# Performance work log

Hardware: AMD Instinct MI355X
Metric: run time of the kernel (lower is better)

The kernel has to match this reference:

```python
import jax, jax.numpy as jnp
import numpy as np

MAX_ITERS = 50
EPS_NORM = 1e-8
EPS_SEP = -1e-6


def setup_inputs() -> dict:
    key = jax.random.key(0)
    k1, k2 = jax.random.split(key)
    pointcloud = jax.random.normal(k1, (200000, 3), dtype=jnp.float32)
    targets = jax.random.normal(k2, (256, 3), dtype=jnp.float32)
    return {"pointcloud": pointcloud, "targets": targets}


def reference(pointcloud, targets):
    # pointcloud: [N, d], targets: [M, d]
    N = pointcloud.shape[0]
    M = targets.shape[0]
    p2 = jnp.sum(pointcloud * pointcloud, axis=1)  # [N]
    t2 = jnp.sum(targets * targets, axis=1)        # [M]

    def step(mask, _):
        # squared euclidean distances [M, N] (argmin identical to cdist argmin)
        d2 = t2[:, None] + p2[None, :] - 2.0 * (targets @ pointcloud.T)
        d2 = jnp.where(mask, d2, jnp.inf)
        closest_idx = jnp.argmin(d2, axis=1)           # [M]
        closest_points = pointcloud[closest_idx]       # [M, d]
        a = closest_points - targets
        a = a / (jnp.linalg.norm(a, axis=1, keepdims=True) + EPS_NORM)
        b = jnp.sum(a * closest_points, axis=1)        # [M]
        dot = a @ pointcloud.T - b[:, None]            # [M, N]
        separated = dot >= EPS_SEP
        mask = mask & ~separated
        return mask, (a, b)

    mask0 = jnp.ones((M, N), dtype=bool)
    _, (a_stack, b_stack) = jax.lax.scan(step, mask0, None, length=MAX_ITERS)
    return a_stack, b_stack  # [MAX_ITERS, M, d], [MAX_ITERS, M]
```

## Files before the change

### kernel.cpp

```cpp
#include <hip/hip_runtime.h>
#include <stdint.h>
#include <math.h>

#pragma clang fp contract(off)

#define BLOCK 1024
#define NW (BLOCK / 64)
#define PT 8
#define PB 4
#define MAX_ITERS 50
#define SOLO_CAP 2048
#define EPS_NORM 1e-8f
#define EPS_SEP (-1e-6f)

__global__ __launch_bounds__(BLOCK) void convex_plane_kernel(
    const float* __restrict__ pc, const float* __restrict__ tg,
    float* __restrict__ out, int N, int M, int CAP, int stepsA)
{
    extern __shared__ uint32_t smem[];
    const int tid  = threadIdx.x;
    const int lane = tid & 63;
    const int wv   = tid >> 6;
    const int m    = blockIdx.x;

    const int maskW = stepsA * (PT * BLOCK / 32);
    uint32_t* mask  = smem;
    int*      list  = (int*)(smem + maskW);
    float*    red_d = (float*)(list + CAP);
    int*      red_i = (int*)(red_d + NW);
    int*      cw    = red_i + NW;
    int*      bcast = cw + NW;
    int*      cnt   = bcast + 2;

    const float tx = tg[3*m+0], ty = tg[3*m+1], tz = tg[3*m+2];
    const float t2 = tx*tx + ty*ty + tz*tz;

    float* out_a = out;
    float* out_b = out + (size_t)MAX_ITERS * (size_t)M * 3;

    auto ldp = [&](int ip, float& x, float& y, float& z) {
        const float* p = pc + 3 * (size_t)ip;
        x = p[0]; y = p[1]; z = p[2];
    };

    auto finish = [&](float dmin, int imin, int mycnt, bool cntFromCursor) -> int2 {
        #pragma unroll
        for (int off = 32; off > 0; off >>= 1) {
            float od = __shfl_down(dmin, off, 64);
            int   oi = __shfl_down(imin, off, 64);
            int   oc = __shfl_down(mycnt, off, 64);
            if (od < dmin || (od == dmin && oi < imin)) { dmin = od; imin = oi; }
            mycnt += oc;
        }
        if (lane == 0) { red_d[wv] = dmin; red_i[wv] = imin; cw[wv] = mycnt; }
        __syncthreads();
        if (wv == 0) {
            float bd = (lane < NW) ? red_d[lane] : INFINITY;
            int   bi = (lane < NW) ? red_i[lane] : 0;
            int   c  = (lane < NW) ? cw[lane]    : 0;
            #pragma unroll
            for (int off = 8; off > 0; off >>= 1) {
                float od = __shfl_down(bd, off, 64);
                int   oi = __shfl_down(bi, off, 64);
                int   oc = __shfl_down(c,  off, 64);
                if (od < bd || (od == bd && oi < bi)) { bd = od; bi = oi; }
                c += oc;
            }
            if (lane == 0) { bcast[0] = bi; bcast[1] = cntFromCursor ? cnt[0] : c; }
        }
        __syncthreads();
        int2 r; r.x = bcast[0]; r.y = bcast[1];
        return r;
    };

    auto scanA = [&](int mode, bool build,
                     float ax, float ay, float az, float b) -> int2 {
        if (tid == 0) cnt[0] = 0;
        __syncthreads();
        float dmin = INFINITY;
        int   imin = 0;
        int   mycnt = 0;
        for (int s = 0; s < stepsA; ++s) {
            const int ib    = s * PT * BLOCK + tid;
            const int wbase = s * (PT * BLOCK / 32);
            uint32_t live = 0;
            if (mode == 2) {
                #pragma unroll
                for (int j = 0; j < PT; ++j) {
                    uint32_t w = mask[wbase + j * (BLOCK / 32) + (tid >> 5)];
                    live |= ((w >> (tid & 31)) & 1u) << j;
                }
            } else {
                #pragma unroll
                for (int j = 0; j < PT; ++j)
                    if (ib + j * BLOCK < N) live |= (1u << j);
            }
            float px[PT], py[PT], pz[PT];
            #pragma unroll
            for (int j = 0; j < PT; ++j) {
                int ip = ib + j * BLOCK;
                ip = ip < N ? ip : N - 1;
                const float* p = pc + 3 * (size_t)ip;
                px[j] = p[0]; py[j] = p[1]; pz[j] = p[2];
            }
            uint32_t keepm = 0;
            #pragma unroll
            for (int j = 0; j < PT; ++j) {
                if ((live >> j) & 1u) {
                    bool keep;
                    if (mode == 0) keep = true;
                    else {
                        float dt = ax*px[j] + ay*py[j] + az*pz[j] - b;
                        keep = (dt < EPS_SEP);
                    }
                    if (keep) {
                        keepm |= (1u << j);
                        float p2 = px[j]*px[j] + py[j]*py[j] + pz[j]*pz[j];
                        float tp = tx*px[j] + ty*py[j] + tz*pz[j];
                        float d2 = t2 + p2 - 2.0f*tp;
                        const int i = ib + j * BLOCK;
                        if (d2 < dmin || (d2 == dmin && i < imin)) {
                            dmin = d2; imin = i;
                        }
                    }
                }
            }
            if (mode != 0) {
                #pragma unroll
                for (int j = 0; j < PT; ++j) {
                    unsigned long long bal = __ballot(((keepm >> j) & 1u) != 0u);
                    const int widx = wbase + j * (BLOCK / 32) + (wv << 1);
                    if (lane == 0)       mask[widx]     = (uint32_t)bal;
                    else if (lane == 32) mask[widx + 1] = (uint32_t)(bal >> 32);
                }
            }
            mycnt += (int)__popc(keepm);
            if (build) {
                int c = (int)__popc(keepm);
                int incl = c;
                #pragma unroll
                for (int off = 1; off < 64; off <<= 1) {
                    int o = __shfl_up(incl, off, 64);
                    if (lane >= off) incl += o;
                }
                const int excl = incl - c;
                const int tot  = __shfl(incl, 63, 64);
                int wb = 0;
                if (lane == 0) wb = atomicAdd(cnt, tot);
                wb = __shfl(wb, 0, 64);
                int pos = wb + excl;
                #pragma unroll
                for (int j = 0; j < PT; ++j) {
                    if ((keepm >> j) & 1u) {
                        if (pos < CAP) list[pos] = ib + j * BLOCK;
                        ++pos;
                    }
                }
            }
        }
        return finish(dmin, imin, mycnt, false);
    };

    auto scanB = [&](int count, float ax, float ay, float az, float b) -> int2 {
        if (tid == 0) cnt[0] = 0;
        __syncthreads();
        float dmin = INFINITY;
        int   imin = 0;
        const int per = BLOCK * PB;
        const int bsteps = (count + per - 1) / per;
        for (int s = 0; s < bsteps; ++s) {
            int jv[PB]; float xv[PB], yv[PB], zv[PB];
            #pragma unroll
            for (int q = 0; q < PB; ++q) {
                int e = s * per + q * BLOCK + tid;
                e = e < count ? e : count - 1;
                jv[q] = list[e];
            }
            #pragma unroll
            for (int q = 0; q < PB; ++q)
                ldp(jv[q], xv[q], yv[q], zv[q]);
            uint32_t keepm = 0;
            float d2v[PB];
            #pragma unroll
            for (int q = 0; q < PB; ++q) {
                const int e = s * per + q * BLOCK + tid;
                if (e < count) {
                    float dt = ax*xv[q] + ay*yv[q] + az*zv[q] - b;
                    if (dt < EPS_SEP) {
                        keepm |= (1u << q);
                        float p2 = xv[q]*xv[q] + yv[q]*yv[q] + zv[q]*zv[q];
                        float tp = tx*xv[q] + ty*yv[q] + tz*zv[q];
                        d2v[q] = t2 + p2 - 2.0f*tp;
                    }
                }
            }
            __syncthreads();
            int c = (int)__popc(keepm);
            int incl = c;
            #pragma unroll
            for (int off = 1; off < 64; off <<= 1) {
                int o = __shfl_up(incl, off, 64);
                if (lane >= off) incl += o;
            }
            const int excl = incl - c;
            const int tot  = __shfl(incl, 63, 64);
            int wb = 0;
            if (lane == 0) wb = atomicAdd(cnt, tot);
            wb = __shfl(wb, 0, 64);
            int pos = wb + excl;
            #pragma unroll
            for (int q = 0; q < PB; ++q) {
                if ((keepm >> q) & 1u) {
                    list[pos] = jv[q];
                    if (d2v[q] < dmin || (d2v[q] == dmin && jv[q] < imin)) {
                        dmin = d2v[q]; imin = jv[q];
                    }
                    ++pos;
                }
            }
        }
        __syncthreads();
        return finish(dmin, imin, 0, true);
    };

    bool comp = false;
    int2 rc = scanA(0, false, 0.f, 0.f, 0.f, 0.f);
    int idx = rc.x, count = rc.y;

    for (int k = 0; k < MAX_ITERS; ++k) {
        if (comp && count <= SOLO_CAP) {
            float* lx = (float*)(list + SOLO_CAP);
            float* ly = lx + SOLO_CAP;
            float* lz = ly + SOLO_CAP;
            for (int e = tid; e < count; e += BLOCK) {
                float x, y, z;
                ldp(list[e], x, y, z);
                lx[e] = x; ly[e] = y; lz[e] = z;
            }
            __syncthreads();
            if (wv != 0) return;
            for (; k < MAX_ITERS; ++k) {
                float cx, cy, cz;
                ldp(idx, cx, cy, cz);
                const float vx = cx - tx, vy = cy - ty, vz = cz - tz;
                const float nrm = sqrtf(vx*vx + vy*vy + vz*vz);
                const float den = nrm + EPS_NORM;
                const float ax = vx / den, ay = vy / den, az = vz / den;
                const float b  = ax*cx + ay*cy + az*cz;
                if (count == 0) {
                    for (int q = lane; q < MAX_ITERS - k; q += 64) {
                        const int kk = k + q;
                        const size_t oa = ((size_t)kk * M + m) * 3;
                        out_a[oa+0] = ax; out_a[oa+1] = ay; out_a[oa+2] = az;
                        out_b[(size_t)kk * M + m] = b;
                    }
                    return;
                }
                if (lane == 0) {
                    const size_t oa = ((size_t)k * M + m) * 3;
                    out_a[oa+0] = ax; out_a[oa+1] = ay; out_a[oa+2] = az;
                    out_b[(size_t)k * M + m] = b;
                }
                if (k + 1 < MAX_ITERS) {
                    float dmin = INFINITY; int imin = 0; int wcur = 0;
                    for (int e0 = 0; e0 < count; e0 += 64) {
                        const int e = e0 + lane;
                        bool keep = false; int j = 0;
                        float d2v = 0.f, px = 0.f, py = 0.f, pz = 0.f;
                        if (e < count) {
                            j = list[e];
                            px = lx[e]; py = ly[e]; pz = lz[e];
                            float dt = ax*px + ay*py + az*pz - b;
                            if (dt < EPS_SEP) {
                                keep = true;
                                float p2 = px*px + py*py + pz*pz;
                                float tp = tx*px + ty*py + tz*pz;
                                d2v = t2 + p2 - 2.0f*tp;
                            }
                        }
                        unsigned long long bal = __ballot(keep);
                        int pos = wcur + (int)__popcll(bal & ((1ull << lane) - 1ull));
                        if (keep) {
                            list[pos] = j;
                            lx[pos] = px; ly[pos] = py; lz[pos] = pz;
                            if (d2v < dmin || (d2v == dmin && j < imin)) {
                                dmin = d2v; imin = j;
                            }
                        }
                        wcur += (int)__popcll(bal);
                    }
                    #pragma unroll
                    for (int off = 32; off > 0; off >>= 1) {
                        float od = __shfl_down(dmin, off, 64);
                        int   oi = __shfl_down(imin, off, 64);
                        if (od < dmin || (od == dmin && oi < imin)) { dmin = od; imin = oi; }
                    }
                    idx = __shfl(imin, 0, 64);
                    count = wcur;
                }
            }
            return;
        }

        float cx, cy, cz;
        ldp(idx, cx, cy, cz);
        const float vx = cx - tx, vy = cy - ty, vz = cz - tz;
        const float nrm = sqrtf(vx*vx + vy*vy + vz*vz);
        const float den = nrm + EPS_NORM;
        const float ax = vx / den, ay = vy / den, az = vz / den;
        const float b  = ax*cx + ay*cy + az*cz;

        if (count == 0) {
            for (int q = tid; q < MAX_ITERS - k; q += BLOCK) {
                const int kk = k + q;
                const size_t oa = ((size_t)kk * M + m) * 3;
                out_a[oa+0] = ax; out_a[oa+1] = ay; out_a[oa+2] = az;
                out_b[(size_t)kk * M + m] = b;
            }
            return;
        }
        if (tid == 0) {
            const size_t oa = ((size_t)k * M + m) * 3;
            out_a[oa+0] = ax; out_a[oa+1] = ay; out_a[oa+2] = az;
            out_b[(size_t)k * M + m] = b;
        }
        if (k + 1 < MAX_ITERS) {
            if (comp) {
                rc = scanB(count, ax, ay, az, b);
            } else {
                const bool build = (count <= (5 * CAP) / 2);
                rc = scanA(k == 0 ? 1 : 2, build, ax, ay, az, b);
                if (build && rc.y <= CAP) comp = true;
            }
            idx = rc.x; count = rc.y;
        }
    }
}

extern "C" void kernel_launch(void* const* d_in, const int* in_sizes, int n_in,
                              void* d_out, int out_size, void* d_ws, size_t ws_size,
                              hipStream_t stream) {
    const float* pc = (const float*)d_in[0];
    const float* tg = (const float*)d_in[1];
    float* out = (float*)d_out;
    const int N = in_sizes[0] / 3;
    const int M = in_sizes[1] / 3;
    const int stepsA = (N + BLOCK * PT - 1) / (BLOCK * PT);
    const size_t maskB  = (size_t)stepsA * (PT * BLOCK / 32) * sizeof(uint32_t);
    const size_t fixedB = NW * (2 * sizeof(int) + sizeof(float)) + 3 * sizeof(int);

    int CAP = 32768;
    size_t smem = maskB + (size_t)CAP * sizeof(int) + fixedB;
    if (hipFuncSetAttribute((const void*)convex_plane_kernel,
                            hipFuncAttributeMaxDynamicSharedMemorySize,
                            (int)smem) != hipSuccess) {
        CAP = 8192;
        smem = maskB + (size_t)CAP * sizeof(int) + fixedB;
    }
    convex_plane_kernel<<<M, BLOCK, smem, stream>>>(pc, tg, out, N, M, CAP, stepsA);
}
```

Measured before the change: 547.5 us.

## Spatially sort points into Morton bins and skip dead wave chunks

Adds preprocessing kernels that histogram the points into a 16^3 Morton-ordered grid, scan the counts and scatter the points into a packed float4 buffer in the workspace, with the original index stored in w. The main kernel reads these packed points, remaps each wave to a contiguous chunk, and records per-chunk survivor counts so later passes skip chunks with no surviving points. Spatial locality should make whole chunks die together under the plane cuts, and the float4 layout gives single vector loads. The cost is several extra launches with atomics and more workspace, and correctness now depends on carrying original indices through for argmin tie-breaking.

```diff
diff --git a/kernel.cpp b/kernel.cpp
--- a/kernel.cpp
+++ b/kernel.cpp
@@ -10,11 +10,92 @@
 #define PB 4
 #define MAX_ITERS 50
 #define SOLO_CAP 2048
+#define NBINS 4096
 #define EPS_NORM 1e-8f
 #define EPS_SEP (-1e-6f)
 
+__device__ __forceinline__ int bin_of(float x, float y, float z) {
+    int cx = (int)floorf((x + 3.5f) * (16.0f / 7.0f));
+    int cy = (int)floorf((y + 3.5f) * (16.0f / 7.0f));
+    int cz = (int)floorf((z + 3.5f) * (16.0f / 7.0f));
+    cx = cx < 0 ? 0 : (cx > 15 ? 15 : cx);
+    cy = cy < 0 ? 0 : (cy > 15 ? 15 : cy);
+    cz = cz < 0 ? 0 : (cz > 15 ? 15 : cz);
+    int code = 0;
+    #pragma unroll
+    for (int b = 0; b < 4; ++b) {
+        code |= ((cx >> b) & 1) << (3 * b);
+        code |= ((cy >> b) & 1) << (3 * b + 1);
+        code |= ((cz >> b) & 1) << (3 * b + 2);
+    }
+    return code;
+}
+
+__global__ void zero_bins(int* __restrict__ binCnt) {
+    const int i = blockIdx.x * blockDim.x + threadIdx.x;
+    if (i < NBINS) binCnt[i] = 0;
+}
+
+__global__ void hist_bins(const float* __restrict__ pc, int* __restrict__ binCnt,
+                          int N) {
+    const int i = blockIdx.x * blockDim.x + threadIdx.x;
+    if (i < N)
+        atomicAdd(&binCnt[bin_of(pc[3*i+0], pc[3*i+1], pc[3*i+2])], 1);
+}
+
+__global__ void scan_bins(const int* __restrict__ binCnt,
+                          int* __restrict__ binCur) {
+    __shared__ int wsum[16];
+    const int t = threadIdx.x, lane = t & 63, wv = t >> 6;
+    const int v0 = binCnt[4*t+0], v1 = binCnt[4*t+1],
+              v2 = binCnt[4*t+2], v3 = binCnt[4*t+3];
+    const int s = v0 + v1 + v2 + v3;
+    int incl = s;
+    #pragma unroll
+    for (int off = 1; off < 64; off <<= 1) {
+        int o = __shfl_up(incl, off, 64);
+        if (lane >= off) incl += o;
+    }
+    if (lane == 63) wsum[wv] = incl;
+    __syncthreads();
+    if (t == 0) {
+        int acc = 0;
+        for (int w = 0; w < 16; ++w) { int x = wsum[w]; wsum[w] = acc; acc += x; }
+    }
+    __syncthreads();
+    const int excl = incl - s + wsum[wv];
+    binCur[4*t+0] = excl;
+    binCur[4*t+1] = excl + v0;
+    binCur[4*t+2] = excl + v0 + v1;
+    binCur[4*t+3] = excl + v0 + v1 + v2;
+}
+
+__global__ void scatter_bins(const float* __restrict__ pc,
+                             float4* __restrict__ pk,
+                             int* __restrict__ binCur, int N) {
+    const int i = blockIdx.x * blockDim.x + threadIdx.x;
+    if (i < N) {
+        const float x = pc[3*i+0], y = pc[3*i+1], z = pc[3*i+2];
+        const int pos = atomicAdd(&binCur[bin_of(x, y, z)], 1);
+        float4 v; v.x = x; v.y = y; v.z = z; v.w = __int_as_float(i);
+        pk[pos] = v;
+    }
+}
+
+__global__ void pack_identity(const float* __restrict__ pc,
+                              float4* __restrict__ pk, int N) {
+    const int i = blockIdx.x * blockDim.x + threadIdx.x;
+    if (i < N) {
+        float4 v; v.x = pc[3*i+0]; v.y = pc[3*i+1]; v.z = pc[3*i+2];
+        v.w = __int_as_float(i);
+        pk[i] = v;
+    }
+}
+
+template <bool PK>
 __global__ __launch_bounds__(BLOCK) void convex_plane_kernel(
-    const float* __restrict__ pc, const float* __restrict__ tg,
+    const float* __restrict__ pc, const float4* __restrict__ pk,
+    const float* __restrict__ tg,
     float* __restrict__ out, int N, int M, int CAP, int stepsA)
 {
     extern __shared__ uint32_t smem[];
@@ -31,17 +112,13 @@
     int*      cw    = red_i + NW;
     int*      bcast = cw + NW;
     int*      cnt   = bcast + 2;
+    int*      chk   = cnt + 1;
 
     const float tx = tg[3*m+0], ty = tg[3*m+1], tz = tg[3*m+2];
     const float t2 = tx*tx + ty*ty + tz*tz;
 
     float* out_a = out;
     float* out_b = out + (size_t)MAX_ITERS * (size_t)M * 3;
-
-    auto ldp = [&](int ip, float& x, float& y, float& z) {
-        const float* p = pc + 3 * (size_t)ip;
-        x = p[0]; y = p[1]; z = p[2];
-    };
 
     auto finish = [&](float dmin, int imin, int mycnt, bool cntFromCursor) -> int2 {
         #pragma unroll
@@ -81,32 +158,46 @@
         int   imin = 0;
         int   mycnt = 0;
         for (int s = 0; s < stepsA; ++s) {
-            const int ib    = s * PT * BLOCK + tid;
-            const int wbase = s * (PT * BLOCK / 32);
-            uint32_t live = 0;
+            const int cid = s * NW + wv;
+            if (mode == 2 && chk[cid] == 0) continue;
+            const int pbase = s * (PT * BLOCK) + wv * (PT * 64) + lane;
+            const int wwb   = s * (PT * BLOCK / 32) + wv * (PT * 2);
+            uint32_t livem = 0;
             if (mode == 2) {
                 #pragma unroll
                 for (int j = 0; j < PT; ++j) {
-                    uint32_t w = mask[wbase + j * (BLOCK / 32) + (tid >> 5)];
-                    live |= ((w >> (tid & 31)) & 1u) << j;
+                    uint32_t w = mask[wwb + j * 2 + (lane >> 5)];
+                    livem |= ((w >> (lane & 31)) & 1u) << j;
                 }
             } else {
                 #pragma unroll
                 for (int j = 0; j < PT; ++j)
-                    if (ib + j * BLOCK < N) live |= (1u << j);
-            }
-            float px[PT], py[PT], pz[PT];
+                    if (pbase + j * 64 < N) livem |= (1u << j);
+            }
+            float px[PT], py[PT], pz[PT]; int ov[PT];
+            if constexpr (PK) {
+                #pragma unroll
+                for (int j = 0; j < PT; ++j) {
+                    int ip = pbase + j * 64;
+                    ip = ip < N ? ip : N - 1;
+                    const float4 v = pk[ip];
+                    px[j] = v.x; py[j] = v.y; pz[j] = v.z;
+                    ov[j] = __float_as_int(v.w);
+                }
+            } else {
+                #pragma unroll
+                for (int j = 0; j < PT; ++j) {
+                    int ip = pbase + j * 64;
+                    ip = ip < N ? ip : N - 1;
+                    const float* p = pc + 3 * (size_t)ip;
+                    px[j] = p[0]; py[j] = p[1]; pz[j] = p[2];
+                    ov[j] = ip;
+                }
+            }
+            uint32_t keepm = 0;
             #pragma unroll
             for (int j = 0; j < PT; ++j) {
-                int ip = ib + j * BLOCK;
-                ip = ip < N ? ip : N - 1;
-                const float* p = pc + 3 * (size_t)ip;
-                px[j] = p[0]; py[j] = p[1]; pz[j] = p[2];
-            }
-            uint32_t keepm = 0;
-            #pragma unroll
-            for (int j = 0; j < PT; ++j) {
-                if ((live >> j) & 1u) {
+                if ((livem >> j) & 1u) {
                     bool keep;
                     if (mode == 0) keep = true;
                     else {
@@ -118,23 +209,26 @@
                         float p2 = px[j]*px[j] + py[j]*py[j] + pz[j]*pz[j];
                         float tp = tx*px[j] + ty*py[j] + tz*pz[j];
                         float d2 = t2 + p2 - 2.0f*tp;
-                        const int i = ib + j * BLOCK;
-                        if (d2 < dmin || (d2 == dmin && i < imin)) {
-                            dmin = d2; imin = i;
+                        if (d2 < dmin || (d2 == dmin && ov[j] < imin)) {
+                            dmin = d2; imin = ov[j];
                         }
                     }
                 }
             }
+            mycnt += (int)__popc(keepm);
             if (mode != 0) {
                 #pragma unroll
                 for (int j = 0; j < PT; ++j) {
                     unsigned long long bal = __ballot(((keepm >> j) & 1u) != 0u);
-                    const int widx = wbase + j * (BLOCK / 32) + (wv << 1);
-                    if (lane == 0)       mask[widx]     = (uint32_t)bal;
-                    else if (lane == 32) mask[widx + 1] = (uint32_t)(bal >> 32);
-                }
-            }
-            mycnt += (int)__popc(keepm);
+                    if (lane == 0)       mask[wwb + j*2]     = (uint32_t)bal;
+                    else if (lane == 32) mask[wwb + j*2 + 1] = (uint32_t)(bal >> 32);
+                }
+                int wsumc = (int)__popc(keepm);
+                #pragma unroll
+                for (int off = 32; off > 0; off >>= 1)
+                    wsumc += __shfl_down(wsumc, off, 64);
+                if (lane == 0) chk[cid] = wsumc;
+            }
             if (build) {
                 int c = (int)__popc(keepm);
                 int incl = c;
@@ -152,7 +246,7 @@
                 #pragma unroll
                 for (int j = 0; j < PT; ++j) {
                     if ((keepm >> j) & 1u) {
-                        if (pos < CAP) list[pos] = ib + j * BLOCK;
+                        if (pos < CAP) list[pos] = pbase + j * 64;
                         ++pos;
                     }
                 }
@@ -169,7 +263,7 @@
         const int per = BLOCK * PB;
         const int bsteps = (count + per - 1) / per;
         for (int s = 0; s < bsteps; ++s) {
-            int jv[PB]; float xv[PB], yv[PB], zv[PB];
+            int jv[PB]; float xv[PB], yv[PB], zv[PB]; int ov[PB]; float d2v[PB];
             #pragma unroll
             for (int q = 0; q < PB; ++q) {
                 int e = s * per + q * BLOCK + tid;
@@ -177,10 +271,18 @@
                 jv[q] = list[e];
             }
             #pragma unroll
-            for (int q = 0; q < PB; ++q)
-                ldp(jv[q], xv[q], yv[q], zv[q]);
+            for (int q = 0; q < PB; ++q) {
+                if constexpr (PK) {
+                    const float4 v = pk[jv[q]];
+                    xv[q] = v.x; yv[q] = v.y; zv[q] = v.z;
+                    ov[q] = __float_as_int(v.w);
+                } else {
+                    const float* p = pc + 3 * (size_t)jv[q];
+                    xv[q] = p[0]; yv[q] = p[1]; zv[q] = p[2];
+                    ov[q] = jv[q];
+                }
+            }
             uint32_t keepm = 0;
-            float d2v[PB];
             #pragma unroll
             for (int q = 0; q < PB; ++q) {
                 const int e = s * per + q * BLOCK + tid;
@@ -212,8 +314,8 @@
             for (int q = 0; q < PB; ++q) {
                 if ((keepm >> q) & 1u) {
                     list[pos] = jv[q];
-                    if (d2v[q] < dmin || (d2v[q] == dmin && jv[q] < imin)) {
-                        dmin = d2v[q]; imin = jv[q];
+                    if (d2v[q] < dmin || (d2v[q] == dmin && ov[q] < imin)) {
+                        dmin = d2v[q]; imin = ov[q];
                     }
                     ++pos;
                 }
@@ -233,15 +335,20 @@
             float* ly = lx + SOLO_CAP;
             float* lz = ly + SOLO_CAP;
             for (int e = tid; e < count; e += BLOCK) {
-                float x, y, z;
-                ldp(list[e], x, y, z);
-                lx[e] = x; ly[e] = y; lz[e] = z;
+                if constexpr (PK) {
+                    const float4 v = pk[list[e]];
+                    lx[e] = v.x; ly[e] = v.y; lz[e] = v.z;
+                    list[e] = __float_as_int(v.w);
+                } else {
+                    const float* p = pc + 3 * (size_t)list[e];
+                    lx[e] = p[0]; ly[e] = p[1]; lz[e] = p[2];
+                }
             }
             __syncthreads();
             if (wv != 0) return;
             for (; k < MAX_ITERS; ++k) {
-                float cx, cy, cz;
-                ldp(idx, cx, cy, cz);
+                const float* cp = pc + 3 * (size_t)idx;
+                const float cx = cp[0], cy = cp[1], cz = cp[2];
                 const float vx = cx - tx, vy = cy - ty, vz = cz - tz;
                 const float nrm = sqrtf(vx*vx + vy*vy + vz*vz);
                 const float den = nrm + EPS_NORM;
@@ -302,8 +409,8 @@
             return;
         }
 
-        float cx, cy, cz;
-        ldp(idx, cx, cy, cz);
+        const float* cp = pc + 3 * (size_t)idx;
+        const float cx = cp[0], cy = cp[1], cz = cp[2];
         const float vx = cx - tx, vy = cy - ty, vz = cz - tz;
         const float nrm = sqrtf(vx*vx + vy*vy + vz*vz);
         const float den = nrm + EPS_NORM;
@@ -347,15 +454,41 @@
     const int M = in_sizes[1] / 3;
     const int stepsA = (N + BLOCK * PT - 1) / (BLOCK * PT);
     const size_t maskB  = (size_t)stepsA * (PT * BLOCK / 32) * sizeof(uint32_t);
-    const size_t fixedB = NW * (2 * sizeof(int) + sizeof(float)) + 3 * sizeof(int);
+    const size_t fixedB = NW * (2 * sizeof(int) + sizeof(float)) + 3 * sizeof(int)
+                        + (size_t)stepsA * NW * sizeof(int);
+    const size_t pkB    = (size_t)N * sizeof(float4);
+    const size_t binB   = 2 * (size_t)NBINS * sizeof(int);
+
+    int wsmode = 0;
+    if (d_ws && ws_size >= pkB + binB) wsmode = 2;
+    else if (d_ws && ws_size >= pkB)   wsmode = 1;
+    float4* pk     = (float4*)d_ws;
+    int*    binCnt = (int*)((char*)d_ws + pkB);
+    int*    binCur = binCnt + NBINS;
 
     int CAP = 32768;
     size_t smem = maskB + (size_t)CAP * sizeof(int) + fixedB;
-    if (hipFuncSetAttribute((const void*)convex_plane_kernel,
-                            hipFuncAttributeMaxDynamicSharedMemorySize,
+    const void* fn = (wsmode >= 1) ? (const void*)convex_plane_kernel<true>
+                                   : (const void*)convex_plane_kernel<false>;
+    if (hipFuncSetAttribute(fn, hipFuncAttributeMaxDynamicSharedMemorySize,
                             (int)smem) != hipSuccess) {
         CAP = 8192;
         smem = maskB + (size_t)CAP * sizeof(int) + fixedB;
     }
-    convex_plane_kernel<<<M, BLOCK, smem, stream>>>(pc, tg, out, N, M, CAP, stepsA);
-}
+    if (wsmode == 2) {
+        const int tpb = 256;
+        zero_bins<<<(NBINS + tpb - 1) / tpb, tpb, 0, stream>>>(binCnt);
+        hist_bins<<<(N + tpb - 1) / tpb, tpb, 0, stream>>>(pc, binCnt, N);
+        scan_bins<<<1, 1024, 0, stream>>>(binCnt, binCur);
+        scatter_bins<<<(N + tpb - 1) / tpb, tpb, 0, stream>>>(pc, pk, binCur, N);
+        convex_plane_kernel<true><<<M, BLOCK, smem, stream>>>(
+            pc, pk, tg, out, N, M, CAP, stepsA);
+    } else if (wsmode == 1) {
+        pack_identity<<<(N + 255) / 256, 256, 0, stream>>>(pc, pk, N);
+        convex_plane_kernel<true><<<M, BLOCK, smem, stream>>>(
+            pc, pk, tg, out, N, M, CAP, stepsA);
+    } else {
+        convex_plane_kernel<false><<<M, BLOCK, smem, stream>>>(
+            pc, nullptr, tg, out, N, M, CAP, stepsA);
+    }
+}
```

Result: slower. 576.7 us (+5.3%).
